# Kernel tuning notes

Measured on AMD Instinct MI355X. Metric: run time of the kernel, lower is better.

Reference implementation:

```python
import jax, jax.numpy as jnp
import numpy as np

SIZE = 1024      # codebook entries
CODE_DIM = 256   # embedding dim


def setup_inputs() -> dict:
    key = jax.random.key(0)
    k_z, k_w = jax.random.split(key)
    z = jax.random.normal(k_z, (8, CODE_DIM, 16, 32, 32), dtype=jnp.float32)
    # init.uniform_(weight, -1/size, 1/size)
    codebook = jax.random.uniform(
        k_w, (SIZE, CODE_DIM), dtype=jnp.float32,
        minval=-1.0 / SIZE, maxval=1.0 / SIZE)
    return {"z": z, "codebook": codebook}


def reference(z, codebook):
    bs, d, t, h, w = z.shape
    # tokens: [N, d] with N = bs*t*h*w (matches permute(0,2,3,4,1).reshape(-1,d))
    zf = jnp.transpose(z, (0, 2, 3, 4, 1)).reshape(-1, d)
    # squared-distance expansion instead of materializing [size, N, d]:
    # ||z - e||^2 = ||z||^2 - 2 z.e + ||e||^2 ; argmin identical to argmin of norm
    d2 = (jnp.sum(zf * zf, axis=1, keepdims=True)
          - 2.0 * (zf @ codebook.T)
          + jnp.sum(codebook * codebook, axis=1))  # [N, size]
    encoding_indices = jnp.argmin(d2, axis=-1).reshape(bs, t, h, w)
    # gather + permute back to [bs, d, t, h, w]
    quantized = jnp.transpose(codebook[encoding_indices], (0, 4, 1, 2, 3))
    st = z + jax.lax.stop_gradient(quantized - z)  # straight-through output
    return (quantized, st, encoding_indices)
```

## Files before the change

kernel.cpp:

```cpp
#include <hip/hip_runtime.h>
#include <stdint.h>


constexpr int Dd  = 256;
constexpr int SPB = 16384;
constexpr int Nn  = 131072;
constexpr int Kk  = 1024;
constexpr int CCAP = 16;
#define WWIN 2.2e-3f

typedef short short8 __attribute__((ext_vector_type(8)));
typedef float v4f    __attribute__((ext_vector_type(4)));

__device__ __forceinline__ unsigned bf16pk(float a, float b){
  unsigned ua = __float_as_uint(a), ub = __float_as_uint(b);
  ua = (ua + 0x7fffu + ((ua >> 16) & 1u)) >> 16;
  ub = (ub + 0x7fffu + ((ub >> 16) & 1u)) & 0xffff0000u;
  return ua | ub;
}
__device__ __forceinline__ short8 frg(uint4 u){
  union { uint4 a; short8 b; } x; x.a = u; return x.b;
}
__device__ __forceinline__ v4f mfma16(short8 a, short8 b, v4f c){
  return __builtin_amdgcn_mfma_f32_16x16x32_bf16(a, b, c, 0, 0, 0);
}
__device__ __forceinline__ void dma16(const void* g, void* l){
  __builtin_amdgcn_global_load_lds((const __attribute__((address_space(1))) void*)g,
                                   (__attribute__((address_space(3))) void*)l, 16, 0, 0);
}

__global__ __launch_bounds__(64) void cnorm_k(const float* __restrict__ cb,
                                              float* __restrict__ cn){
  const int k = blockIdx.x, l = threadIdx.x;
  const float* row = cb + (size_t)k * Dd;
  float s = 0.f;
  #pragma unroll
  for (int c = 0; c < Dd; c += 64){ float v = row[c + l]; s += v * v; }
  #pragma unroll
  for (int off = 32; off > 0; off >>= 1) s += __shfl_down(s, off, 64);
  if (l == 0) cn[k] = s;
}

__global__ __launch_bounds__(256) void cconv_k(const float* __restrict__ cb,
                                               uint4* __restrict__ Bg){
  const int cc = blockIdx.x, n = threadIdx.x;
  const float* row = cb + (size_t)(cc * 256 + n) * Dd;
  for (int dc = 0; dc < 8; dc++){
    float v[32];
    const float4* rp = (const float4*)(row + dc * 32);
    #pragma unroll
    for (int q = 0; q < 8; q++){
      float4 f = rp[q]; v[4*q]=f.x; v[4*q+1]=f.y; v[4*q+2]=f.z; v[4*q+3]=f.w;
    }
    unsigned hv[16];
    #pragma unroll
    for (int p = 0; p < 16; p++) hv[p] = bf16pk(v[2*p], v[2*p+1]);
    size_t base = ((size_t)cc * 8 + dc) * 1024;
    #pragma unroll
    for (int kq = 0; kq < 4; kq++)
      Bg[base + (size_t)kq*256 + n] = make_uint4(hv[4*kq],hv[4*kq+1],hv[4*kq+2],hv[4*kq+3]);
  }
}

__device__ __forceinline__ void epi(const v4f (&acc)[4], const int c,
                                    const int li, const int lq, const int w,
                                    const int tok0, const float* cnS,
                                    unsigned (&bestR)[4], unsigned (&thrU)[4],
                                    int (&cntR)[4],
                                    unsigned short* __restrict__ candW){
  float cnv[4];
  #pragma unroll
  for (int ni = 0; ni < 4; ni++) cnv[ni] = cnS[c*64 + ni*16 + li];
  const int codeB = c*64 + li;
  #pragma unroll
  for (int r = 0; r < 4; r++){
    unsigned pv[4];
    unsigned pm = 0xFFFFFFFFu;
    #pragma unroll
    for (int ni = 0; ni < 4; ni++){
      float s = fmaf(acc[ni][r], -2.0f, cnv[ni]);
      unsigned u = __float_as_uint(s);
      u ^= (unsigned)((int)u >> 31) | 0x80000000u;
      unsigned p = (u & 0xFFFFFC00u) | (unsigned)(codeB + ni*16);
      pv[ni] = p;
      pm = (pm < p) ? pm : p;
    }
    unsigned pmw = pm;
    #pragma unroll
    for (int off = 1; off < 16; off <<= 1){
      unsigned o = (unsigned)__shfl_xor((int)pmw, off, 16);
      pmw = (pmw < o) ? pmw : o;
    }
    if (pmw <= bestR[r]){
      bestR[r] = pmw;
      unsigned bp = pmw & 0xFFFFFC00u;
      unsigned fb = (bp & 0x80000000u) ? (bp ^ 0x80000000u) : ~bp;
      float thrf = __uint_as_float(fb) + WWIN;
      unsigned tu = __float_as_uint(thrf);
      tu ^= (unsigned)((int)tu >> 31) | 0x80000000u;
      thrU[r] = tu | 1023u;
    }
    if (__any(pm <= thrU[r])){
      const int tok = tok0 + w*16 + lq*4 + r;
      int base = cntR[r];
      #pragma unroll
      for (int ni = 0; ni < 4; ni++){
        const unsigned p = pv[ni];
        const bool pass = (p <= thrU[r]);
        unsigned long long bal = __ballot(pass);
        const unsigned bq = (unsigned)(bal >> (lq*16)) & 0xFFFFu;
        if (pass){
          int pos = base + __popc(bq & ((1u << li) - 1u));
          if (pos < CCAP)
            candW[(size_t)tok*CCAP + pos] = (unsigned short)(p & 1023u);
        }
        base += __popc(bq);
      }
      cntR[r] = base;
    }
  }
}

__global__ __launch_bounds__(512, 4) void vq_sweep_k(const float* __restrict__ z,
                                                     const uint4* __restrict__ Bg,
                                                     const float* __restrict__ cnG,
                                                     int* __restrict__ cntW,
                                                     unsigned short* __restrict__ candW,
                                                     int* __restrict__ abestW,
                                                     int* __restrict__ idsW,
                                                     float* __restrict__ out){
  __shared__ uint4 Bs[2][2048];
  __shared__ float cnS[1024];

  const int tid = threadIdx.x, bId = blockIdx.x;
  const int w = tid >> 6, ln = tid & 63;
  const int li = ln & 15, lq = ln >> 4;

  if (w < 4) dma16((const uint4*)cnG + w*64 + ln, (uint4*)&cnS[w*256]);
  int bOff[4];
  #pragma unroll
  for (int j = 0; j < 4; j++){
    const int f = j*512 + tid;
    bOff[j] = (f >> 8)*1024 + ((f >> 6) & 3)*256 + (f & 63);
  }
  #pragma unroll
  for (int j = 0; j < 4; j++)
    dma16(Bg + bOff[j], &Bs[0][j*512 + w*64]);

  const int tok0 = bId * 128;
  const int b = tok0 >> 14;
  const int s0 = tok0 & 16383;
  const float* zb = z + (size_t)b * Dd * SPB + s0;
  short8 aF[8];
  const int tl = w*16 + li;
  #pragma unroll
  for (int kk = 0; kk < 8; kk++){
    float v[8];
    #pragma unroll
    for (int j = 0; j < 8; j++)
      v[j] = zb[(size_t)(kk*32 + lq*8 + j) * SPB + tl];
    union { unsigned u[4]; short8 s8; } x;
    #pragma unroll
    for (int p = 0; p < 4; p++) x.u[p] = bf16pk(v[2*p], v[2*p+1]);
    aF[kk] = x.s8;
  }

  unsigned bestR[4], thrU[4]; int cntR[4];
  #pragma unroll
  for (int i = 0; i < 4; i++){ bestR[i] = 0xFFFFFFFFu; thrU[i] = 0u; cntR[i] = 0; }

  v4f accA[4], accB[4];
  const v4f vz = {0.f, 0.f, 0.f, 0.f};

  for (int cp = 0; cp < 8; cp++){
    const int c0 = cp*2, c1 = c0 + 1;

    {
      const int cn1 = c0 + 1;
      const int srcB = (cn1 >> 2)*8192 + (cn1 & 3)*64;
      #pragma unroll
      for (int j = 0; j < 4; j++)
        dma16(Bg + srcB + bOff[j], &Bs[1][j*512 + w*64]);
      asm volatile("s_waitcnt vmcnt(4)" ::: "memory");
      __builtin_amdgcn_s_barrier();
      asm volatile("" ::: "memory");

      #pragma unroll
      for (int ni = 0; ni < 4; ni++) accA[ni] = vz;
      const uint4* Bbase = &Bs[0][lq*64 + li];
      __builtin_amdgcn_s_setprio(1);
      #pragma unroll
      for (int kk = 0; kk < 8; kk++){
        short8 b0 = frg(Bbase[kk*256 +  0]);
        short8 b1 = frg(Bbase[kk*256 + 16]);
        short8 b2 = frg(Bbase[kk*256 + 32]);
        short8 b3 = frg(Bbase[kk*256 + 48]);
        accA[0] = mfma16(aF[kk], b0, accA[0]);
        accA[1] = mfma16(aF[kk], b1, accA[1]);
        accA[2] = mfma16(aF[kk], b2, accA[2]);
        accA[3] = mfma16(aF[kk], b3, accA[3]);
      }
      __builtin_amdgcn_s_setprio(0);
      if (cp)
        epi(accB, c0 - 1, li, lq, w, tok0, cnS, bestR, thrU, cntR, candW);
      __builtin_amdgcn_s_barrier();
      asm volatile("" ::: "memory");
    }

    {
      if (c1 < 15){
        const int cn1 = c1 + 1;
        const int srcB = (cn1 >> 2)*8192 + (cn1 & 3)*64;
        #pragma unroll
        for (int j = 0; j < 4; j++)
          dma16(Bg + srcB + bOff[j], &Bs[0][j*512 + w*64]);
        asm volatile("s_waitcnt vmcnt(4)" ::: "memory");
      } else {
        asm volatile("s_waitcnt vmcnt(0)" ::: "memory");
      }
      __builtin_amdgcn_s_barrier();
      asm volatile("" ::: "memory");

      #pragma unroll
      for (int ni = 0; ni < 4; ni++) accB[ni] = vz;
      const uint4* Bbase = &Bs[1][lq*64 + li];
      __builtin_amdgcn_s_setprio(1);
      #pragma unroll
      for (int kk = 0; kk < 8; kk++){
        short8 b0 = frg(Bbase[kk*256 +  0]);
        short8 b1 = frg(Bbase[kk*256 + 16]);
        short8 b2 = frg(Bbase[kk*256 + 32]);
        short8 b3 = frg(Bbase[kk*256 + 48]);
        accB[0] = mfma16(aF[kk], b0, accB[0]);
        accB[1] = mfma16(aF[kk], b1, accB[1]);
        accB[2] = mfma16(aF[kk], b2, accB[2]);
        accB[3] = mfma16(aF[kk], b3, accB[3]);
      }
      __builtin_amdgcn_s_setprio(0);
      epi(accA, c0, li, lq, w, tok0, cnS, bestR, thrU, cntR, candW);
      __builtin_amdgcn_s_barrier();
      asm volatile("" ::: "memory");
    }
  }
  epi(accB, 15, li, lq, w, tok0, cnS, bestR, thrU, cntR, candW);

  if (li == 0){
    #pragma unroll
    for (int r = 0; r < 4; r++){
      const int tok = tok0 + w*16 + lq*4 + r;
      cntW[tok] = cntR[r];
      if (cntR[r] == 1){
        const int code = (int)(bestR[r] & 1023u);
        idsW[tok] = code;
        out[(size_t)2 * Nn * Dd + tok] = (float)code;
      } else {
        abestW[tok] = (int)(bestR[r] & 1023u);
      }
    }
  }
}

__global__ __launch_bounds__(256) void vq_finish_k(const float* __restrict__ z,
                                                   const float* __restrict__ cb,
                                                   const float* __restrict__ cnG,
                                                   const int* __restrict__ cntW,
                                                   const unsigned short* __restrict__ candW,
                                                   const int* __restrict__ abestW,
                                                   const int* __restrict__ idsW,
                                                   float* __restrict__ out){
  __shared__ __align__(16) float smem[64*129];
  __shared__ int idS[128];
  __shared__ int anyH;

  const int tid = threadIdx.x, reg = blockIdx.x;
  const int tok0 = reg * 128;
  const int b = tok0 >> 14, sb = tok0 & 16383;

  if (tid == 0) anyH = 0;
  int cntL = 0;
  if (tid < 128){
    idS[tid] = idsW[tok0 + tid];
    cntL = cntW[tok0 + tid];
  }
  __syncthreads();
  const bool act = (cntL > 1);
  if (act) anyH = 1;
  __syncthreads();

  if (anyH){
    float* zS = smem;
    const float* zb = z + (size_t)b * Dd * SPB + sb;

    const int tok = tok0 + tid;
    const int tl = tid;
    int n = 0, abest = 0;
    bool ovf = false;
    unsigned short cds[CCAP];
    if (act){
      n = cntL;
      ovf = (n > CCAP);
      if (ovf) n = CCAP;
      *(uint4*)&cds[0] = *(const uint4*)&candW[(size_t)tok * CCAP];
      *(uint4*)&cds[8] = *(const uint4*)&candW[(size_t)tok * CCAP + 8];
      abest = abestW[tok];
    }
    const int eIdx = act ? (ovf ? abest : (int)cds[0]) : 0;

    float accs[CCAP];
    #pragma unroll
    for (int i = 0; i < CCAP; i++) accs[i] = 0.f;
    float accE = 0.f, za = 0.f;

    for (int ch = 0; ch < 4; ch++){
      if (ch) __syncthreads();
      #pragma unroll
      for (int rr = 0; rr < 8; rr++){
        const int f4 = rr*256 + tid;
        const int row = f4 >> 5, c4 = f4 & 31;
        const float4 v = *(const float4*)(zb + (size_t)(ch*64 + row) * SPB + c4*4);
        *(float4*)&zS[row*128 + c4*4] = v;
      }
      __syncthreads();
      if (act){
        #pragma unroll 8
        for (int d = 0; d < 64; d++){
          const float v = zS[d*128 + tl];
          za = fmaf(v, v, za);
        }
        #pragma unroll
        for (int ci = 0; ci < CCAP; ci++){
          if (ci < n){
            const float* cr = cb + (size_t)cds[ci] * Dd + ch*64;
            float a = accs[ci];
            #pragma unroll
            for (int d = 0; d < 64; d += 4){
              const float4 cv = *(const float4*)(cr + d);
              a = fmaf(zS[(d+0)*128 + tl], cv.x, a);
              a = fmaf(zS[(d+1)*128 + tl], cv.y, a);
              a = fmaf(zS[(d+2)*128 + tl], cv.z, a);
              a = fmaf(zS[(d+3)*128 + tl], cv.w, a);
            }
            accs[ci] = a;
          }
        }
        if (ovf){
          const float* cr = cb + (size_t)eIdx * Dd + ch*64;
          float a = accE;
          #pragma unroll
          for (int d = 0; d < 64; d += 4){
            const float4 cv = *(const float4*)(cr + d);
            a = fmaf(zS[(d+0)*128 + tl], cv.x, a);
            a = fmaf(zS[(d+1)*128 + tl], cv.y, a);
            a = fmaf(zS[(d+2)*128 + tl], cv.z, a);
            a = fmaf(zS[(d+3)*128 + tl], cv.w, a);
          }
          accE = a;
        }
      }
    }

    if (act){
      float bv = 3.4e38f; int bi = 0x7fffffff;
      #pragma unroll
      for (int ci = 0; ci < CCAP; ci++){
        if (ci < n){
          const int ix = (int)cds[ci];
          float t  = za - 2.0f * accs[ci];
          float d2 = t + cnG[ix];
          if (d2 < bv || (d2 == bv && ix < bi)){ bv = d2; bi = ix; }
        }
      }
      if (ovf){
        float t  = za - 2.0f * accE;
        float d2 = t + cnG[eIdx];
        if (d2 < bv || (d2 == bv && eIdx < bi)){ bv = d2; bi = eIdx; }
      }
      idS[tl] = bi;
      out[(size_t)2 * Nn * Dd + tok] = (float)bi;
    }
  }
  __syncthreads();

  float* tile = smem;
  const int r2 = tid >> 7, ccol = tid & 127;
  const int s4 = tid & 15, d16 = tid >> 4;
  for (int hh = 0; hh < 2; hh++){
    const int s0h = hh * 64;
    float* qb  = out + (size_t)b * Dd * SPB + sb + s0h + s4*4;
    float* stb = qb + (size_t)Nn * Dd;
    for (int ch = 0; ch < 2; ch++){
      if (hh | ch) __syncthreads();
      #pragma unroll 4
      for (int t0 = 0; t0 < 64; t0 += 2){
        const int row = t0 + r2;
        tile[row*129 + ccol] = cb[(size_t)idS[s0h + row] * Dd + ch*128 + ccol];
      }
      __syncthreads();
      #pragma unroll
      for (int k = 0; k < 8; k++){
        const int dcol = d16 + 16*k;
        float4 v;
        v.x = tile[(s4*4 + 0)*129 + dcol];
        v.y = tile[(s4*4 + 1)*129 + dcol];
        v.z = tile[(s4*4 + 2)*129 + dcol];
        v.w = tile[(s4*4 + 3)*129 + dcol];
        const size_t off = (size_t)(ch*128 + dcol) * SPB;
        *(float4*)(qb  + off) = v;
        *(float4*)(stb + off) = v;
      }
    }
  }
}

#define MICRO_STEP(WITH_ZN)                                                    \
    {                                                                          \
        float4 a0 = *(const float4*)&As[d][ty * 8];                            \
        float4 a1 = *(const float4*)&As[d][ty * 8 + 4];                        \
        float4 b0 = *(const float4*)&Bs[d][tx * 8];                            \
        float4 b1 = *(const float4*)&Bs[d][tx * 8 + 4];                        \
        float a[8] = {a0.x, a0.y, a0.z, a0.w, a1.x, a1.y, a1.z, a1.w};         \
        float bb[8] = {b0.x, b0.y, b0.z, b0.w, b1.x, b1.y, b1.z, b1.w};        \
        _Pragma("unroll")                                                      \
        for (int i = 0; i < 8; i++) {                                          \
            _Pragma("unroll")                                                  \
            for (int j = 0; j < 8; j++) acc[i][j] += a[i] * bb[j];             \
            if (WITH_ZN) zn[i] += a[i] * a[i];                                 \
        }                                                                      \
    }

__global__ __launch_bounds__(256) void vq_k(const float* __restrict__ z,
                                            const float* __restrict__ cb,
                                            const float* __restrict__ cn,
                                            float* __restrict__ out){
  __shared__ float As[16][128];
  __shared__ float Bs[16][132];
  __shared__ int   idsf[128];
  const int tid = threadIdx.x;
  const int tx = tid & 15, ty = tid >> 4;
  const int blk = blockIdx.x;
  const int b = blk >> 7, sb = (blk & 127) * 128;
  const float* zb = z + (size_t)b * Dd * SPB + sb;
  float bestv[8]; int besti[8]; float zn[8];
  #pragma unroll
  for (int i = 0; i < 8; i++){ bestv[i] = 3.4e38f; besti[i] = 0; zn[i] = 0.f; }
  const int am = tid & 127, ad = tid >> 7;
  const int bd = tid & 15,  bk = tid >> 4;
  for (int cc = 0; cc < 8; cc++){
    float acc[8][8];
    #pragma unroll
    for (int i = 0; i < 8; i++)
      #pragma unroll
      for (int j = 0; j < 8; j++) acc[i][j] = 0.f;
    for (int dc = 0; dc < 16; dc++){
      #pragma unroll
      for (int r = 0; r < 8; r++){
        const int d = ad + r * 2;
        As[d][am] = zb[(size_t)(dc*16 + d) * SPB + am];
      }
      #pragma unroll
      for (int r = 0; r < 8; r++){
        const int k = bk + r * 16;
        Bs[bd][k] = cb[(size_t)(cc*128 + k) * Dd + dc*16 + bd];
      }
      __syncthreads();
      if (cc == 0){
        #pragma unroll
        for (int d = 0; d < 16; d++) MICRO_STEP(1)
      } else {
        #pragma unroll
        for (int d = 0; d < 16; d++) MICRO_STEP(0)
      }
      __syncthreads();
    }
    const float* cnp = cn + cc*128 + tx*8;
    float4 c0 = *(const float4*)cnp;
    float4 c1 = *(const float4*)(cnp + 4);
    float cv[8] = {c0.x, c0.y, c0.z, c0.w, c1.x, c1.y, c1.z, c1.w};
    #pragma unroll
    for (int i = 0; i < 8; i++){
      #pragma unroll
      for (int j = 0; j < 8; j++){
        float t  = zn[i] - 2.0f * acc[i][j];
        float d2 = t + cv[j];
        int   ix = cc*128 + tx*8 + j;
        if (d2 < bestv[i]){ bestv[i] = d2; besti[i] = ix; }
      }
    }
  }
  #pragma unroll
  for (int i = 0; i < 8; i++){
    float v = bestv[i]; int ix = besti[i];
    #pragma unroll
    for (int off = 8; off > 0; off >>= 1){
      float ov = __shfl_down(v, off, 16);
      int   oi = __shfl_down(ix, off, 16);
      if (ov < v || (ov == v && oi < ix)){ v = ov; ix = oi; }
    }
    if (tx == 0) idsf[ty*8 + i] = ix;
  }
  __syncthreads();
  if (tid < 128) out[(size_t)2*Nn*Dd + (size_t)blk*128 + tid] = (float)idsf[tid];
  const int m = tid & 127, cg = tid >> 7;
  const int myidx = idsf[m];
  const float* crow = cb + (size_t)myidx * Dd + cg*128;
  float* q  = out + (size_t)b * Dd * SPB + (size_t)cg * 128 * SPB + sb + m;
  float* st = q + (size_t)Nn * Dd;
  #pragma unroll 8
  for (int r = 0; r < 128; r++){
    const float v = crow[r];
    q[(size_t)r * SPB]  = v;
    st[(size_t)r * SPB] = v;
  }
}

extern "C" void kernel_launch(void* const* d_in, const int* in_sizes, int n_in,
                              void* d_out, int out_size, void* d_ws, size_t ws_size,
                              hipStream_t stream){
  const float* z  = (const float*)d_in[0];
  const float* cb = (const float*)d_in[1];
  float* out = (float*)d_out;

  const size_t BG_B  = (size_t)4 * 8 * 1024 * 16;
  const size_t CN_B  = (size_t)Kk * 4;
  const size_t CNT_B = (size_t)Nn * 4;
  const size_t CAN_B = (size_t)Nn * CCAP * 2;
  const size_t ABW_B = (size_t)Nn * 4;
  const size_t IDS_B = (size_t)Nn * 4;
  const size_t NEED = BG_B + CN_B + CNT_B + CAN_B + ABW_B + IDS_B;

  if (ws_size >= NEED){
    uint8_t* ws = (uint8_t*)d_ws;
    size_t o = 0;
    uint4* Bg   = (uint4*)(ws + o);          o += BG_B;
    float* cnG  = (float*)(ws + o);          o += CN_B;
    int*   cntW = (int*)(ws + o);            o += CNT_B;
    unsigned short* candW = (unsigned short*)(ws + o); o += CAN_B;
    int*   abW  = (int*)(ws + o);            o += ABW_B;
    int*   idsW = (int*)(ws + o);            o += IDS_B;

    cnorm_k<<<Kk, 64, 0, stream>>>(cb, cnG);
    cconv_k<<<4, 256, 0, stream>>>(cb, Bg);
    vq_sweep_k<<<Nn/128, 512, 0, stream>>>(z, Bg, cnG, cntW, candW, abW,
                                           idsW, out);
    vq_finish_k<<<Nn/128, 256, 0, stream>>>(z, cb, cnG, cntW, candW, abW,
                                            idsW, out);
  } else {
    float* cn = (float*)d_ws;
    cnorm_k<<<Kk, 64, 0, stream>>>(cb, cn);
    vq_k<<<Nn/128, 256, 0, stream>>>(z, cb, cn, out);
  }
}
```

Measured before the change: 593.6 us.

## Fuse candidate refinement into sweep kernel and gather outputs from transposed codebook

Candidate lists, counts and approximate best indices now stay in shared memory, and the exact fp32 refinement runs inside the sweep kernel. This removes the global workspace round-trip and the separate finish kernel. The output writes move to a new kernel that loads a transposed codebook slice into LDS and gathers per token, so quantized and straight-through rows are written as coalesced float4 stores. This adds a codebook transpose in cconv_k and extra LDS use in the sweep kernel, which may reduce occupancy.

New measurement: 655.2 us. +10.4%, slower.

```diff
diff --git a/kernel.cpp b/kernel.cpp
--- a/kernel.cpp
+++ b/kernel.cpp
@@ -42,7 +42,8 @@
 }
 
 __global__ __launch_bounds__(256) void cconv_k(const float* __restrict__ cb,
-                                               uint4* __restrict__ Bg){
+                                               uint4* __restrict__ Bg,
+                                               float* __restrict__ cbT){
   const int cc = blockIdx.x, n = threadIdx.x;
   const float* row = cb + (size_t)(cc * 256 + n) * Dd;
   for (int dc = 0; dc < 8; dc++){
@@ -52,6 +53,9 @@
     for (int q = 0; q < 8; q++){
       float4 f = rp[q]; v[4*q]=f.x; v[4*q+1]=f.y; v[4*q+2]=f.z; v[4*q+3]=f.w;
     }
+    #pragma unroll
+    for (int j = 0; j < 32; j++)
+      cbT[(size_t)(dc*32 + j) * 1024 + cc*256 + n] = v[j];
     unsigned hv[16];
     #pragma unroll
     for (int p = 0; p < 16; p++) hv[p] = bf16pk(v[2*p], v[2*p+1]);
@@ -64,10 +68,10 @@
 
 __device__ __forceinline__ void epi(const v4f (&acc)[4], const int c,
                                     const int li, const int lq, const int w,
-                                    const int tok0, const float* cnS,
+                                    const float* cnS,
                                     unsigned (&bestR)[4], unsigned (&thrU)[4],
                                     int (&cntR)[4],
-                                    unsigned short* __restrict__ candW){
+                                    unsigned short* __restrict__ candL){
   float cnv[4];
   #pragma unroll
   for (int ni = 0; ni < 4; ni++) cnv[ni] = cnS[c*64 + ni*16 + li];
@@ -101,7 +105,7 @@
       thrU[r] = tu | 1023u;
     }
     if (__any(pm <= thrU[r])){
-      const int tok = tok0 + w*16 + lq*4 + r;
+      const int row = w*16 + lq*4 + r;
       int base = cntR[r];
       #pragma unroll
       for (int ni = 0; ni < 4; ni++){
@@ -112,7 +116,7 @@
         if (pass){
           int pos = base + __popc(bq & ((1u << li) - 1u));
           if (pos < CCAP)
-            candW[(size_t)tok*CCAP + pos] = (unsigned short)(p & 1023u);
+            candL[row*CCAP + pos] = (unsigned short)(p & 1023u);
         }
         base += __popc(bq);
       }
@@ -122,19 +126,24 @@
 }
 
 __global__ __launch_bounds__(512, 4) void vq_sweep_k(const float* __restrict__ z,
+                                                     const float* __restrict__ cb,
                                                      const uint4* __restrict__ Bg,
                                                      const float* __restrict__ cnG,
-                                                     int* __restrict__ cntW,
-                                                     unsigned short* __restrict__ candW,
-                                                     int* __restrict__ abestW,
                                                      int* __restrict__ idsW,
                                                      float* __restrict__ out){
   __shared__ uint4 Bs[2][2048];
   __shared__ float cnS[1024];
+  __shared__ uint4 candU[128][2];
+  __shared__ int cntS[128];
+  __shared__ int abS[128];
+  __shared__ int anyH;
+  unsigned short* candL = (unsigned short*)candU;
 
   const int tid = threadIdx.x, bId = blockIdx.x;
   const int w = tid >> 6, ln = tid & 63;
   const int li = ln & 15, lq = ln >> 4;
+
+  if (tid == 0) anyH = 0;
 
   if (w < 4) dma16((const uint4*)cnG + w*64 + ln, (uint4*)&cnS[w*256]);
   int bOff[4];
@@ -152,13 +161,13 @@
   const int s0 = tok0 & 16383;
   const float* zb = z + (size_t)b * Dd * SPB + s0;
   short8 aF[8];
-  const int tl = w*16 + li;
+  const int tl8 = w*16 + li;
   #pragma unroll
   for (int kk = 0; kk < 8; kk++){
     float v[8];
     #pragma unroll
     for (int j = 0; j < 8; j++)
-      v[j] = zb[(size_t)(kk*32 + lq*8 + j) * SPB + tl];
+      v[j] = zb[(size_t)(kk*32 + lq*8 + j) * SPB + tl8];
     union { unsigned u[4]; short8 s8; } x;
     #pragma unroll
     for (int p = 0; p < 4; p++) x.u[p] = bf16pk(v[2*p], v[2*p+1]);
@@ -202,7 +211,7 @@
       }
       __builtin_amdgcn_s_setprio(0);
       if (cp)
-        epi(accB, c0 - 1, li, lq, w, tok0, cnS, bestR, thrU, cntR, candW);
+        epi(accB, c0 - 1, li, lq, w, cnS, bestR, thrU, cntR, candL);
       __builtin_amdgcn_s_barrier();
       asm volatile("" ::: "memory");
     }
@@ -237,62 +246,37 @@
         accB[3] = mfma16(aF[kk], b3, accB[3]);
       }
       __builtin_amdgcn_s_setprio(0);
-      epi(accA, c0, li, lq, w, tok0, cnS, bestR, thrU, cntR, candW);
+      epi(accA, c0, li, lq, w, cnS, bestR, thrU, cntR, candL);
       __builtin_amdgcn_s_barrier();
       asm volatile("" ::: "memory");
     }
   }
-  epi(accB, 15, li, lq, w, tok0, cnS, bestR, thrU, cntR, candW);
+  epi(accB, 15, li, lq, w, cnS, bestR, thrU, cntR, candL);
 
   if (li == 0){
     #pragma unroll
     for (int r = 0; r < 4; r++){
-      const int tok = tok0 + w*16 + lq*4 + r;
-      cntW[tok] = cntR[r];
+      const int row = w*16 + lq*4 + r;
+      const int tok = tok0 + row;
+      cntS[row] = cntR[r];
+      abS[row]  = (int)(bestR[r] & 1023u);
       if (cntR[r] == 1){
         const int code = (int)(bestR[r] & 1023u);
         idsW[tok] = code;
         out[(size_t)2 * Nn * Dd + tok] = (float)code;
       } else {
-        abestW[tok] = (int)(bestR[r] & 1023u);
-      }
-    }
-  }
-}
-
-__global__ __launch_bounds__(256) void vq_finish_k(const float* __restrict__ z,
-                                                   const float* __restrict__ cb,
-                                                   const float* __restrict__ cnG,
-                                                   const int* __restrict__ cntW,
-                                                   const unsigned short* __restrict__ candW,
-                                                   const int* __restrict__ abestW,
-                                                   const int* __restrict__ idsW,
-                                                   float* __restrict__ out){
-  __shared__ __align__(16) float smem[64*129];
-  __shared__ int idS[128];
-  __shared__ int anyH;
-
-  const int tid = threadIdx.x, reg = blockIdx.x;
-  const int tok0 = reg * 128;
-  const int b = tok0 >> 14, sb = tok0 & 16383;
-
-  if (tid == 0) anyH = 0;
-  int cntL = 0;
-  if (tid < 128){
-    idS[tid] = idsW[tok0 + tid];
-    cntL = cntW[tok0 + tid];
+        anyH = 1;
+      }
+    }
   }
   __syncthreads();
-  const bool act = (cntL > 1);
-  if (act) anyH = 1;
-  __syncthreads();
 
   if (anyH){
-    float* zS = smem;
-    const float* zb = z + (size_t)b * Dd * SPB + sb;
-
-    const int tok = tok0 + tid;
+    float* zS = (float*)&Bs[0][0];
     const int tl = tid;
+    const int cntL = (tid < 128) ? cntS[tid] : 0;
+    const bool act = (cntL > 1);
+    const int tok = tok0 + tl;
     int n = 0, abest = 0;
     bool ovf = false;
     unsigned short cds[CCAP];
@@ -300,9 +284,9 @@
       n = cntL;
       ovf = (n > CCAP);
       if (ovf) n = CCAP;
-      *(uint4*)&cds[0] = *(const uint4*)&candW[(size_t)tok * CCAP];
-      *(uint4*)&cds[8] = *(const uint4*)&candW[(size_t)tok * CCAP + 8];
-      abest = abestW[tok];
+      *(uint4*)&cds[0] = candU[tl][0];
+      *(uint4*)&cds[8] = candU[tl][1];
+      abest = abS[tl];
     }
     const int eIdx = act ? (ovf ? abest : (int)cds[0]) : 0;
 
@@ -314,8 +298,8 @@
     for (int ch = 0; ch < 4; ch++){
       if (ch) __syncthreads();
       #pragma unroll
-      for (int rr = 0; rr < 8; rr++){
-        const int f4 = rr*256 + tid;
+      for (int rr = 0; rr < 4; rr++){
+        const int f4 = rr*512 + tid;
         const int row = f4 >> 5, c4 = f4 & 31;
         const float4 v = *(const float4*)(zb + (size_t)(ch*64 + row) * SPB + c4*4);
         *(float4*)&zS[row*128 + c4*4] = v;
@@ -366,48 +350,51 @@
         if (ci < n){
           const int ix = (int)cds[ci];
           float t  = za - 2.0f * accs[ci];
-          float d2 = t + cnG[ix];
+          float d2 = t + cnS[ix];
           if (d2 < bv || (d2 == bv && ix < bi)){ bv = d2; bi = ix; }
         }
       }
       if (ovf){
         float t  = za - 2.0f * accE;
-        float d2 = t + cnG[eIdx];
+        float d2 = t + cnS[eIdx];
         if (d2 < bv || (d2 == bv && eIdx < bi)){ bv = d2; bi = eIdx; }
       }
-      idS[tl] = bi;
+      idsW[tok] = bi;
       out[(size_t)2 * Nn * Dd + tok] = (float)bi;
     }
   }
+}
+
+__global__ __launch_bounds__(256) void vq_out_k(const float* __restrict__ cbT,
+                                                const int* __restrict__ idsW,
+                                                float* __restrict__ out){
+  __shared__ float rows[8*1024];
+  __shared__ int   idsS[2048];
+  const int tid = threadIdx.x, blk = blockIdx.x;
+  const int b = blk >> 8, dg = (blk >> 3) & 31, sc = blk & 7;
+
+  const float4* src = (const float4*)(cbT + (size_t)dg*8*1024);
+  #pragma unroll
+  for (int r = 0; r < 8; r++)
+    ((float4*)rows)[r*256 + tid] = src[r*256 + tid];
+  const int4* ip = (const int4*)(idsW + (size_t)b*SPB + sc*2048);
+  ((int4*)idsS)[tid]       = ip[tid];
+  ((int4*)idsS)[256 + tid] = ip[256 + tid];
   __syncthreads();
 
-  float* tile = smem;
-  const int r2 = tid >> 7, ccol = tid & 127;
-  const int s4 = tid & 15, d16 = tid >> 4;
-  for (int hh = 0; hh < 2; hh++){
-    const int s0h = hh * 64;
-    float* qb  = out + (size_t)b * Dd * SPB + sb + s0h + s4*4;
-    float* stb = qb + (size_t)Nn * Dd;
-    for (int ch = 0; ch < 2; ch++){
-      if (hh | ch) __syncthreads();
-      #pragma unroll 4
-      for (int t0 = 0; t0 < 64; t0 += 2){
-        const int row = t0 + r2;
-        tile[row*129 + ccol] = cb[(size_t)idS[s0h + row] * Dd + ch*128 + ccol];
-      }
-      __syncthreads();
-      #pragma unroll
-      for (int k = 0; k < 8; k++){
-        const int dcol = d16 + 16*k;
-        float4 v;
-        v.x = tile[(s4*4 + 0)*129 + dcol];
-        v.y = tile[(s4*4 + 1)*129 + dcol];
-        v.z = tile[(s4*4 + 2)*129 + dcol];
-        v.w = tile[(s4*4 + 3)*129 + dcol];
-        const size_t off = (size_t)(ch*128 + dcol) * SPB;
-        *(float4*)(qb  + off) = v;
-        *(float4*)(stb + off) = v;
-      }
+  #pragma unroll
+  for (int d = 0; d < 8; d++){
+    float* q  = out + (size_t)(b*256 + dg*8 + d) * SPB + sc*2048;
+    float* st = q + (size_t)Nn * Dd;
+    const float* rd = rows + d*1024;
+    #pragma unroll
+    for (int k = 0; k < 2; k++){
+      const int p = k*256 + tid;
+      const int4 iv = ((const int4*)idsS)[p];
+      float4 v;
+      v.x = rd[iv.x]; v.y = rd[iv.y]; v.z = rd[iv.z]; v.w = rd[iv.w];
+      ((float4*)q)[p]  = v;
+      ((float4*)st)[p] = v;
     }
   }
 }
@@ -522,28 +509,22 @@
 
   const size_t BG_B  = (size_t)4 * 8 * 1024 * 16;
   const size_t CN_B  = (size_t)Kk * 4;
-  const size_t CNT_B = (size_t)Nn * 4;
-  const size_t CAN_B = (size_t)Nn * CCAP * 2;
-  const size_t ABW_B = (size_t)Nn * 4;
+  const size_t CBT_B = (size_t)Dd * Kk * 4;
   const size_t IDS_B = (size_t)Nn * 4;
-  const size_t NEED = BG_B + CN_B + CNT_B + CAN_B + ABW_B + IDS_B;
+  const size_t NEED = BG_B + CN_B + CBT_B + IDS_B;
 
   if (ws_size >= NEED){
     uint8_t* ws = (uint8_t*)d_ws;
     size_t o = 0;
     uint4* Bg   = (uint4*)(ws + o);          o += BG_B;
     float* cnG  = (float*)(ws + o);          o += CN_B;
-    int*   cntW = (int*)(ws + o);            o += CNT_B;
-    unsigned short* candW = (unsigned short*)(ws + o); o += CAN_B;
-    int*   abW  = (int*)(ws + o);            o += ABW_B;
+    float* cbT  = (float*)(ws + o);          o += CBT_B;
     int*   idsW = (int*)(ws + o);            o += IDS_B;
 
     cnorm_k<<<Kk, 64, 0, stream>>>(cb, cnG);
-    cconv_k<<<4, 256, 0, stream>>>(cb, Bg);
-    vq_sweep_k<<<Nn/128, 512, 0, stream>>>(z, Bg, cnG, cntW, candW, abW,
-                                           idsW, out);
-    vq_finish_k<<<Nn/128, 256, 0, stream>>>(z, cb, cnG, cntW, candW, abW,
-                                            idsW, out);
+    cconv_k<<<4, 256, 0, stream>>>(cb, Bg, cbT);
+    vq_sweep_k<<<Nn/128, 512, 0, stream>>>(z, cb, Bg, cnG, idsW, out);
+    vq_out_k<<<Nn/64, 256, 0, stream>>>(cbT, idsW, out);
   } else {
     float* cn = (float*)d_ws;
     cnorm_k<<<Kk, 64, 0, stream>>>(cb, cn);
```
